# Optimization experiments

Measured on AMD Instinct MI355X. Metric: run time of the kernel, lower is better.

Reference implementation:

```python
import jax, jax.numpy as jnp
import numpy as np

D_MODEL = 1024
N_HEADS = 16
HEAD_DIM = D_MODEL // N_HEADS
B, S = 2, 2048


def setup_inputs() -> dict:
    key = jax.random.key(0)
    ks = jax.random.split(key, 12)
    sd = 1.0 / np.sqrt(D_MODEL)
    inp = {
        "x": jax.random.normal(ks[0], (B, S, D_MODEL), dtype=jnp.float32),
        "rel_bias": jax.random.normal(ks[1], (N_HEADS, S, S), dtype=jnp.float32) * 0.02,
        "attn_mask": jnp.zeros((1, 1, S, S), dtype=jnp.float32),
        # Linear params in torch layout: W [out, in], b [out]
        "Wq": jax.random.normal(ks[2], (D_MODEL, D_MODEL), dtype=jnp.float32) * sd,
        "bq": jnp.zeros((D_MODEL,), dtype=jnp.float32),
        "Wk": jax.random.normal(ks[3], (D_MODEL, D_MODEL), dtype=jnp.float32) * sd,
        "bk": jnp.zeros((D_MODEL,), dtype=jnp.float32),
        "Wv": jax.random.normal(ks[4], (D_MODEL, D_MODEL), dtype=jnp.float32) * sd,
        "bv": jnp.zeros((D_MODEL,), dtype=jnp.float32),
        "Wo": jax.random.normal(ks[5], (D_MODEL, D_MODEL), dtype=jnp.float32) * sd,
        "bo": jnp.zeros((D_MODEL,), dtype=jnp.float32),
    }
    return inp


def _split_heads(t):
    # [B, S, D] -> [B, H, S, Hd]
    b, s, _ = t.shape
    return t.reshape(b, s, N_HEADS, HEAD_DIM).transpose(0, 2, 1, 3)


def reference(x, rel_bias, attn_mask, Wq, bq, Wk, bk, Wv, bv, Wo, bo):
    scale = HEAD_DIM ** (-0.5)
    q = _split_heads(x @ Wq.T + bq)  # [B, H, S, Hd]
    k = _split_heads(x @ Wk.T + bk)
    v = _split_heads(x @ Wv.T + bv)
    scores = jnp.einsum("bhqd,bhkd->bhqk", q, k) * scale
    scores = scores + rel_bias  # [H,S,S] broadcasts over batch
    scores = scores + attn_mask  # [1,1,S,S]
    probs = jax.nn.softmax(scores, axis=-1)
    ctx = jnp.einsum("bhqk,bhkd->bhqd", probs, v)  # [B, H, S, Hd]
    ctx = ctx.transpose(0, 2, 1, 3).reshape(x.shape[0], x.shape[1], D_MODEL)
    return ctx @ Wo.T + bo
```

## Files before the change

### kernel.cpp

```cpp
#include <hip/hip_runtime.h>
#include <hip/hip_bf16.h>
#include <stdint.h>

#define S_LEN 2048
#define DM 1024
#define NH 16
#define HD 64

typedef __bf16 bf16x8 __attribute__((ext_vector_type(8)));
typedef float f32x4 __attribute__((ext_vector_type(4)));
typedef unsigned short u16x4 __attribute__((ext_vector_type(4)));

#if __has_builtin(__builtin_amdgcn_exp2f)
#define EXP2F(x) __builtin_amdgcn_exp2f(x)
#else
#define EXP2F(x) exp2f(x)
#endif

__device__ __forceinline__ unsigned short f2bf(float f){
  union { float f; uint32_t u; } v; v.f = f;
  uint32_t r = v.u + 0x7fffu + ((v.u >> 16) & 1u);
  return (unsigned short)(r >> 16);
}

__device__ __forceinline__ float bf2f(unsigned short u){
  union { uint32_t u; float f; } v; v.u = ((uint32_t)u) << 16;
  return v.f;
}

__device__ __forceinline__ void load_lds16(const void* g, void* l){
  __builtin_amdgcn_global_load_lds((const __attribute__((address_space(1))) void*)g,
                                   (__attribute__((address_space(3))) void*)l, 16, 0, 0);
}

__device__ __forceinline__ f32x4 mfma16(bf16x8 a, bf16x8 b, f32x4 c){
  return __builtin_amdgcn_mfma_f32_16x16x32_bf16(a, b, c, 0, 0, 0);
}

__device__ __forceinline__ bf16x8 lds_swz_read(const unsigned short* base, int row, int cb){
  int addr = (row << 7) + (cb ^ ((row & 7) << 4));
  return *reinterpret_cast<const bf16x8*>(reinterpret_cast<const char*>(base) + addr);
}

__global__ void prep_kernel(const float* __restrict__ x,
                            const float* __restrict__ wq, const float* __restrict__ wk,
                            const float* __restrict__ wv, const float* __restrict__ wo,
                            unsigned short* __restrict__ ws_base){
  long idx = ((long)blockIdx.x * 256 + threadIdx.x) * 4;
  const float* s; unsigned short* d; long off;
  if (idx < (1L << 22)) { s = x; d = ws_base; off = idx; }
  else {
    long r = idx - (1L << 22);
    int wsel = (int)(r >> 20);
    off = r & ((1L << 20) - 1);
    s = wsel == 0 ? wq : wsel == 1 ? wk : wsel == 2 ? wv : wo;
    d = ws_base + (1L << 22) + ((long)wsel << 20);
  }
  float4 f = *reinterpret_cast<const float4*>(s + off);
  u16x4 o;
  o[0] = f2bf(f.x); o[1] = f2bf(f.y); o[2] = f2bf(f.z); o[3] = f2bf(f.w);
  *reinterpret_cast<u16x4*>(d + off) = o;
}

template<int MODE>
__global__ __launch_bounds__(256, 2)
void gemm_bt_kernel(const unsigned short* __restrict__ A,
                    const unsigned short* __restrict__ B0,
                    const unsigned short* __restrict__ B1,
                    const unsigned short* __restrict__ B2,
                    const float* __restrict__ bias0,
                    const float* __restrict__ bias1,
                    const float* __restrict__ bias2,
                    unsigned short* __restrict__ q_out,
                    unsigned short* __restrict__ k_out,
                    unsigned short* __restrict__ vt_out,
                    float* __restrict__ f_out)
{
  __shared__ unsigned short As[128 * 64];
  __shared__ unsigned short Bs[128 * 64];
  const int tid = threadIdx.x;
  const int lane = tid & 63;
  const int w = tid >> 6;
  const int wr = w >> 1, wc = w & 1;
  const int mBase = blockIdx.y * 128;
  int nb = blockIdx.x;
  const unsigned short* Bmat; const float* bias; int mat;
  if constexpr (MODE == 0) {
    mat = nb >> 3;
    nb &= 7;
    Bmat = mat == 0 ? B0 : (mat == 1 ? B1 : B2);
    bias = mat == 0 ? bias0 : (mat == 1 ? bias1 : bias2);
  } else { mat = 0; Bmat = B0; bias = bias0; }
  const int nBase = nb * 128;

  f32x4 acc[4][4] = {};
  const int srow = lane >> 3;
  const int ksrc = ((lane & 7) ^ srow) * 8;
  const unsigned short* ArowBase = A    + (size_t)(mBase + w * 32 + srow) * DM + ksrc;
  const unsigned short* BrowBase = Bmat + (size_t)(nBase + w * 32 + srow) * DM + ksrc;

  for (int kt = 0; kt < 16; ++kt) {
    #pragma unroll
    for (int i = 0; i < 4; ++i) {
      load_lds16(ArowBase + (size_t)(i * 8) * DM + kt * 64, &As[(w * 4 + i) * 512]);
      load_lds16(BrowBase + (size_t)(i * 8) * DM + kt * 64, &Bs[(w * 4 + i) * 512]);
    }
    __syncthreads();
    #pragma unroll
    for (int kk = 0; kk < 2; ++kk) {
      bf16x8 af[4], bfr[4];
      const int cb = kk * 64 + ((lane >> 4) << 4);
      #pragma unroll
      for (int m = 0; m < 4; ++m)
        af[m] = lds_swz_read(As, wr * 64 + m * 16 + (lane & 15), cb);
      #pragma unroll
      for (int n = 0; n < 4; ++n)
        bfr[n] = lds_swz_read(Bs, wc * 64 + n * 16 + (lane & 15), cb);
      #pragma unroll
      for (int m = 0; m < 4; ++m)
        #pragma unroll
        for (int n = 0; n < 4; ++n)
          acc[m][n] = mfma16(af[m], bfr[n], acc[m][n]);
    }
    __syncthreads();
  }

  #pragma unroll
  for (int m = 0; m < 4; ++m) {
    #pragma unroll
    for (int n = 0; n < 4; ++n) {
      const int col = nBase + wc * 64 + n * 16 + (lane & 15);
      const float bv = bias[col];
      const int row0 = mBase + wr * 64 + m * 16 + ((lane >> 4) << 2);
      if constexpr (MODE == 1) {
        #pragma unroll
        for (int j = 0; j < 4; ++j)
          f_out[(size_t)(row0 + j) * DM + col] = acc[m][n][j] + bv;
      } else {
        const int h = col >> 6, d = col & 63;
        if (mat < 2) {
          unsigned short* dst = (mat == 0) ? q_out : k_out;
          #pragma unroll
          for (int j = 0; j < 4; ++j) {
            const int row = row0 + j;
            const int b = row >> 11, s = row & 2047;
            dst[(((size_t)b * NH + h) * S_LEN + s) * HD + d] = f2bf(acc[m][n][j] + bv);
          }
        } else {
          const int b = row0 >> 11, s = row0 & 2047;
          u16x4 pk;
          #pragma unroll
          for (int j = 0; j < 4; ++j) pk[j] = f2bf(acc[m][n][j] + bv);
          *reinterpret_cast<u16x4*>(&vt_out[(((size_t)b * NH + h) * HD + d) * S_LEN + s]) = pk;
        }
      }
    }
  }
}


#define WAITV8 do { asm volatile("s_waitcnt vmcnt(8)" ::: "memory"); } while (0)
#define WAITV2 do { asm volatile("s_waitcnt vmcnt(2)" ::: "memory"); } while (0)
#define WAITV0 do { asm volatile("s_waitcnt vmcnt(0)" ::: "memory"); } while (0)
#define SB0    __builtin_amdgcn_sched_barrier(0)
#define BAR    __builtin_amdgcn_s_barrier()

#define LOAD_RAW(lB) do {                                                              \
    rb0 = *reinterpret_cast<const f32x4*>(bpB + (size_t)(0  + rg) * S_LEN + (lB) + cl4); \
    rb1 = *reinterpret_cast<const f32x4*>(bpB + (size_t)(4  + rg) * S_LEN + (lB) + cl4); \
    rb2 = *reinterpret_cast<const f32x4*>(bpB + (size_t)(8  + rg) * S_LEN + (lB) + cl4); \
    rb3 = *reinterpret_cast<const f32x4*>(bpB + (size_t)(12 + rg) * S_LEN + (lB) + cl4); \
    rm0 = *reinterpret_cast<const f32x4*>(mpB + (size_t)(0  + rg) * S_LEN + (lB) + cl4); \
    rm1 = *reinterpret_cast<const f32x4*>(mpB + (size_t)(4  + rg) * S_LEN + (lB) + cl4); \
    rm2 = *reinterpret_cast<const f32x4*>(mpB + (size_t)(8  + rg) * S_LEN + (lB) + cl4); \
    rm3 = *reinterpret_cast<const f32x4*>(mpB + (size_t)(12 + rg) * S_LEN + (lB) + cl4); \
  } while (0)

#define COMBINE do {                                                                   \
    f32x4 c0_ = (rb0 + rm0) * L2E; f32x4 c1_ = (rb1 + rm1) * L2E;                      \
    f32x4 c2_ = (rb2 + rm2) * L2E; f32x4 c3_ = (rb3 + rm3) * L2E;                      \
    u16x4 p0_, p1_, p2_, p3_;                                                          \
    p0_[0]=f2bf(c0_[0]); p0_[1]=f2bf(c0_[1]); p0_[2]=f2bf(c0_[2]); p0_[3]=f2bf(c0_[3]);\
    p1_[0]=f2bf(c1_[0]); p1_[1]=f2bf(c1_[1]); p1_[2]=f2bf(c1_[2]); p1_[3]=f2bf(c1_[3]);\
    p2_[0]=f2bf(c2_[0]); p2_[1]=f2bf(c2_[1]); p2_[2]=f2bf(c2_[2]); p2_[3]=f2bf(c2_[3]);\
    p3_[0]=f2bf(c3_[0]); p3_[1]=f2bf(c3_[1]); p3_[2]=f2bf(c3_[2]); p3_[3]=f2bf(c3_[3]);\
    char* Pb_ = reinterpret_cast<char*>(Pw_);                                          \
    *reinterpret_cast<u16x4*>(Pb_ + ((0  + rg) << 7) + (cl8 ^ ((0 + rg) << 4))) = p0_; \
    *reinterpret_cast<u16x4*>(Pb_ + ((4  + rg) << 7) + (cl8 ^ ((4 + rg) << 4))) = p1_; \
    *reinterpret_cast<u16x4*>(Pb_ + ((8  + rg) << 7) + (cl8 ^ ((0 + rg) << 4))) = p2_; \
    *reinterpret_cast<u16x4*>(Pb_ + ((12 + rg) << 7) + (cl8 ^ ((4 + rg) << 4))) = p3_; \
    bm0 = *reinterpret_cast<const u16x4*>(Pb_ + (q << 7) + ((0 * 32 + g * 8) ^ qx_));  \
    bm1 = *reinterpret_cast<const u16x4*>(Pb_ + (q << 7) + ((1 * 32 + g * 8) ^ qx_));  \
    bm2 = *reinterpret_cast<const u16x4*>(Pb_ + (q << 7) + ((2 * 32 + g * 8) ^ qx_));  \
    bm3 = *reinterpret_cast<const u16x4*>(Pb_ + (q << 7) + ((3 * 32 + g * 8) ^ qx_));  \
  } while (0)

#define STAGE_K(kvB) \
    load_lds16(Kp + (size_t)((kvB) + w * 8 + srow) * HD + ksrc, &Ks[w * 512])

#define STAGE_V(kvB) \
    load_lds16(Vp + (size_t)(w * 8 + srow) * S_LEN + (kvB) + ksrc, &Vs[w * 512])

#define BIAS_COL(SCN, BMN) do {                                               \
    SCN[0] = SCN[0] * SC + bf2f(BMN[0]);                                      \
    SCN[1] = SCN[1] * SC + bf2f(BMN[1]);                                      \
    SCN[2] = SCN[2] * SC + bf2f(BMN[2]);                                      \
    SCN[3] = SCN[3] * SC + bf2f(BMN[3]);                                      \
    mt_ = fmaxf(mt_, fmaxf(fmaxf(SCN[0], SCN[1]), fmaxf(SCN[2], SCN[3])));    \
  } while (0)

#define EXP_COL(SCN) do {                                                     \
    SCN[0] = EXP2F(SCN[0] - mn_); SCN[1] = EXP2F(SCN[1] - mn_);               \
    SCN[2] = EXP2F(SCN[2] - mn_); SCN[3] = EXP2F(SCN[3] - mn_);               \
  } while (0)

#define PWR_COL(NN, SCN) do {                                                 \
    u16x4 pk_;                                                                \
    pk_[0] = f2bf(SCN[0]); pk_[1] = f2bf(SCN[1]);                             \
    pk_[2] = f2bf(SCN[2]); pk_[3] = f2bf(SCN[3]);                             \
    const int colb_ = ((NN) * 16 + 4 * g) * 2;                                \
    *reinterpret_cast<u16x4*>(                                                \
        reinterpret_cast<char*>(Pw_) + (q << 7) + (colb_ ^ ((q & 7) << 4))) = pk_; \
  } while (0)

#define COMPUTE_TILE do {                                                     \
    f32x4 sc0_, sc1_, sc2_, sc3_;                                             \
    { bf16x8 a_ = lds_swz_read(Ks, 0 * 16 + q, cbq);                          \
      bf16x8 b_ = lds_swz_read(Ks, 0 * 16 + q, 64 + cbq);                     \
      f32x4 z_ = {}; z_ = mfma16(a_, qf0, z_); sc0_ = mfma16(b_, qf1, z_); }  \
    { bf16x8 a_ = lds_swz_read(Ks, 1 * 16 + q, cbq);                          \
      bf16x8 b_ = lds_swz_read(Ks, 1 * 16 + q, 64 + cbq);                     \
      f32x4 z_ = {}; z_ = mfma16(a_, qf0, z_); sc1_ = mfma16(b_, qf1, z_); }  \
    { bf16x8 a_ = lds_swz_read(Ks, 2 * 16 + q, cbq);                          \
      bf16x8 b_ = lds_swz_read(Ks, 2 * 16 + q, 64 + cbq);                     \
      f32x4 z_ = {}; z_ = mfma16(a_, qf0, z_); sc2_ = mfma16(b_, qf1, z_); }  \
    { bf16x8 a_ = lds_swz_read(Ks, 3 * 16 + q, cbq);                          \
      bf16x8 b_ = lds_swz_read(Ks, 3 * 16 + q, 64 + cbq);                     \
      f32x4 z_ = {}; z_ = mfma16(a_, qf0, z_); sc3_ = mfma16(b_, qf1, z_); }  \
    float mt_ = -3.0e38f;                                                     \
    BIAS_COL(sc0_, bm0); BIAS_COL(sc1_, bm1);                                 \
    BIAS_COL(sc2_, bm2); BIAS_COL(sc3_, bm3);                                 \
    mt_ = fmaxf(mt_, __shfl_xor(mt_, 16));                                    \
    mt_ = fmaxf(mt_, __shfl_xor(mt_, 32));                                    \
    const float mn_ = fmaxf(m_run, mt_);                                      \
    const float corr_ = EXP2F(m_run - mn_);                                   \
    m_run = mn_;                                                              \
    EXP_COL(sc0_); EXP_COL(sc1_); EXP_COL(sc2_); EXP_COL(sc3_);               \
    f32x4 ls4_ = sc0_ + sc1_ + sc2_ + sc3_;                                   \
    float ls_ = ls4_[0] + ls4_[1] + ls4_[2] + ls4_[3];                        \
    ls_ += __shfl_xor(ls_, 16);                                               \
    ls_ += __shfl_xor(ls_, 32);                                               \
    l_run = l_run * corr_ + ls_;                                              \
    acc0_ *= corr_; acc1_ *= corr_; acc2_ *= corr_; acc3_ *= corr_;           \
    PWR_COL(0, sc0_); PWR_COL(1, sc1_); PWR_COL(2, sc2_); PWR_COL(3, sc3_);   \
    bf16x8 pf0_ = lds_swz_read(Pw_, q, cbq);                                  \
    bf16x8 pf1_ = lds_swz_read(Pw_, q, 64 + cbq);                             \
    { bf16x8 a_ = lds_swz_read(Vs, 0 * 16 + q, cbq);                          \
      bf16x8 b_ = lds_swz_read(Vs, 0 * 16 + q, 64 + cbq);                     \
      acc0_ = mfma16(a_, pf0_, acc0_); acc0_ = mfma16(b_, pf1_, acc0_); }     \
    { bf16x8 a_ = lds_swz_read(Vs, 1 * 16 + q, cbq);                          \
      bf16x8 b_ = lds_swz_read(Vs, 1 * 16 + q, 64 + cbq);                     \
      acc1_ = mfma16(a_, pf0_, acc1_); acc1_ = mfma16(b_, pf1_, acc1_); }     \
    { bf16x8 a_ = lds_swz_read(Vs, 2 * 16 + q, cbq);                          \
      bf16x8 b_ = lds_swz_read(Vs, 2 * 16 + q, 64 + cbq);                     \
      acc2_ = mfma16(a_, pf0_, acc2_); acc2_ = mfma16(b_, pf1_, acc2_); }     \
    { bf16x8 a_ = lds_swz_read(Vs, 3 * 16 + q, cbq);                          \
      bf16x8 b_ = lds_swz_read(Vs, 3 * 16 + q, 64 + cbq);                     \
      acc3_ = mfma16(a_, pf0_, acc3_); acc3_ = mfma16(b_, pf1_, acc3_); }     \
  } while (0)

__global__ __launch_bounds__(512) __attribute__((amdgpu_waves_per_eu(4, 5)))
void attn_kernel(const unsigned short* __restrict__ Q,
                 const unsigned short* __restrict__ Kmat,
                 const unsigned short* __restrict__ Vt,
                 const float* __restrict__ rel_bias,
                 const float* __restrict__ mask,
                 unsigned short* __restrict__ ctxp0,
                 unsigned short* __restrict__ ctxp1,
                 unsigned short* __restrict__ ctxp2,
                 unsigned short* __restrict__ ctxp3,
                 float* __restrict__ Mbuf,
                 float* __restrict__ Lbuf)
{
  __shared__ unsigned short Ks[64 * 64];
  __shared__ unsigned short Vs[64 * 64];
  __shared__ unsigned short Ps[8][16 * 64];

  const int logical = (blockIdx.x & 7) * 256 + (blockIdx.x >> 3);
  const int s  = logical & 3;
  const int b  = (logical >> 2) & 1;
  const int qt = (logical >> 3) & 15;
  const int h  = logical >> 7;

  const int lane = threadIdx.x & 63, w = threadIdx.x >> 6;
  const int q = lane & 15, g = lane >> 4;
  const int bh = b * NH + h;
  const int qRow = qt * 128 + w * 16;
  const int kv0 = s << 9;
  const unsigned short* Qp = Q + ((size_t)bh * S_LEN + qRow) * HD;
  bf16x8 qf0 = *reinterpret_cast<const bf16x8*>(Qp + (size_t)q * HD + g * 8);
  bf16x8 qf1 = *reinterpret_cast<const bf16x8*>(Qp + (size_t)q * HD + 32 + g * 8);

  const unsigned short* Kp = Kmat + (size_t)bh * S_LEN * HD;
  const unsigned short* Vp = Vt + (size_t)bh * HD * S_LEN;
  const float* bpB = rel_bias + (size_t)h * S_LEN * S_LEN + (size_t)qRow * S_LEN + kv0;
  const float* mpB = mask + (size_t)qRow * S_LEN + kv0;

  float m_run = -3.0e38f, l_run = 0.f;
  f32x4 acc0_ = {}, acc1_ = {}, acc2_ = {}, acc3_ = {};
  f32x4 rb0, rb1, rb2, rb3, rm0, rm1, rm2, rm3;
  u16x4 bm0, bm1, bm2, bm3;

  const float SC  = 0.125f * 1.44269504089f;
  const float L2E = 1.44269504089f;

  const int srow = lane >> 3;
  const int ksrc = ((lane & 7) ^ srow) * 8;
  const int cbq = g << 4;
  const int rg  = lane >> 4;
  const int cl4 = (lane & 15) * 4;
  const int cl8 = (lane & 15) * 8;
  const int qx_ = (q & 7) << 4;
  unsigned short* Pw_ = Ps[w];

  LOAD_RAW(0);
  SB0;

  for (int t = 0; t < 7; ++t) {
    const int kvB = kv0 + t * 64;
    BAR;
    STAGE_K(kvB); STAGE_V(kvB);
    SB0;
    WAITV2; SB0;
    COMBINE;
    LOAD_RAW((t + 1) * 64);
    SB0;
    WAITV8; SB0;
    BAR;
    COMPUTE_TILE;
  }
  {
    const int kvB = kv0 + 7 * 64;
    BAR;
    STAGE_K(kvB); STAGE_V(kvB);
    SB0;
    WAITV2; SB0;
    COMBINE;
    WAITV0; SB0;
    BAR;
    COMPUTE_TILE;
  }

  const float inv = 1.0f / l_run;
  acc0_ *= inv; acc1_ *= inv; acc2_ *= inv; acc3_ *= inv;
  PWR_COL(0, acc0_); PWR_COL(1, acc1_); PWR_COL(2, acc2_); PWR_COL(3, acc3_);
  bf16x8 c0 = lds_swz_read(Pw_, q, g << 4);
  bf16x8 c1 = lds_swz_read(Pw_, q, 64 + (g << 4));
  unsigned short* pbase = (s == 0) ? ctxp0 : (s == 1) ? ctxp1 : (s == 2) ? ctxp2 : ctxp3;
  unsigned short* cp = pbase + ((size_t)(b * S_LEN + qRow + q)) * DM + h * HD;
  *reinterpret_cast<bf16x8*>(cp + 8 * g) = c0;
  *reinterpret_cast<bf16x8*>(cp + 32 + 8 * g) = c1;
  if (g == 0) {
    const int mlIdx = (s << 16) + (bh << 11) + qRow + q;
    Mbuf[mlIdx] = m_run;
    Lbuf[mlIdx] = l_run;
  }
}

__global__ void merge_kernel(const unsigned short* __restrict__ ctxp0,
                             const unsigned short* __restrict__ ctxp1,
                             const unsigned short* __restrict__ ctxp2,
                             const unsigned short* __restrict__ ctxp3,
                             const float* __restrict__ Mbuf,
                             const float* __restrict__ Lbuf,
                             unsigned short* __restrict__ ctx){
  const long e = ((long)blockIdx.x * 256 + threadIdx.x) * 4;
  const int b = (int)(e >> 21);
  const int srow = (int)((e >> 10) & 2047);
  const int d = (int)(e & 1023);
  const int h = d >> 6;
  const int idx = ((b * NH + h) << 11) + srow;
  const float m0 = Mbuf[idx],               m1 = Mbuf[(1 << 16) + idx];
  const float m2 = Mbuf[(2 << 16) + idx],   m3 = Mbuf[(3 << 16) + idx];
  const float l0 = Lbuf[idx],               l1 = Lbuf[(1 << 16) + idx];
  const float l2 = Lbuf[(2 << 16) + idx],   l3 = Lbuf[(3 << 16) + idx];
  const float mm = fmaxf(fmaxf(m0, m1), fmaxf(m2, m3));
  const float w0 = EXP2F(m0 - mm) * l0;
  const float w1 = EXP2F(m1 - mm) * l1;
  const float w2 = EXP2F(m2 - mm) * l2;
  const float w3 = EXP2F(m3 - mm) * l3;
  const float inv = 1.0f / (w0 + w1 + w2 + w3);
  u16x4 c0 = *reinterpret_cast<const u16x4*>(ctxp0 + e);
  u16x4 c1 = *reinterpret_cast<const u16x4*>(ctxp1 + e);
  u16x4 c2 = *reinterpret_cast<const u16x4*>(ctxp2 + e);
  u16x4 c3 = *reinterpret_cast<const u16x4*>(ctxp3 + e);
  u16x4 o;
  #pragma unroll
  for (int j = 0; j < 4; ++j)
    o[j] = f2bf((bf2f(c0[j]) * w0 + bf2f(c1[j]) * w1 +
                 bf2f(c2[j]) * w2 + bf2f(c3[j]) * w3) * inv);
  *reinterpret_cast<u16x4*>(ctx + e) = o;
}

extern "C" void kernel_launch(void* const* d_in, const int* in_sizes, int n_in,
                              void* d_out, int out_size, void* d_ws, size_t ws_size,
                              hipStream_t stream) {
  (void)in_sizes; (void)n_in; (void)out_size; (void)ws_size;
  const float* x  = (const float*)d_in[0];
  const float* rb = (const float*)d_in[1];
  const float* mk = (const float*)d_in[2];
  const float* Wq = (const float*)d_in[3];
  const float* bq = (const float*)d_in[4];
  const float* Wk = (const float*)d_in[5];
  const float* bk = (const float*)d_in[6];
  const float* Wv = (const float*)d_in[7];
  const float* bv = (const float*)d_in[8];
  const float* Wo = (const float*)d_in[9];
  const float* bo = (const float*)d_in[10];
  float* out = (float*)d_out;

  unsigned short* ws  = (unsigned short*)d_ws;
  unsigned short* xb  = ws;
  unsigned short* wqb = ws + (1L << 22);
  unsigned short* wkb = wqb + (1L << 20);
  unsigned short* wvb = wkb + (1L << 20);
  unsigned short* wob = wvb + (1L << 20);
  unsigned short* Qw  = wob + (1L << 20);
  unsigned short* Kw  = Qw + (1L << 22);
  unsigned short* Vtw = Kw + (1L << 22);
  unsigned short* ctx = Vtw + (1L << 22);
  unsigned short* ctxp1 = xb;
  unsigned short* ctxp2 = (unsigned short*)d_out;
  unsigned short* ctxp3 = (unsigned short*)d_out + (1L << 22);
  float* Mb = (float*)wqb;
  float* Lb = (float*)(wqb + (1L << 19));

  prep_kernel<<<8192, 256, 0, stream>>>(x, Wq, Wk, Wv, Wo, ws);
  gemm_bt_kernel<0><<<dim3(24, 32), 256, 0, stream>>>(
      xb, wqb, wkb, wvb, bq, bk, bv, Qw, Kw, Vtw, nullptr);
  attn_kernel<<<2048, 512, 0, stream>>>(Qw, Kw, Vtw, rb, mk, ctx, ctxp1, ctxp2, ctxp3, Mb, Lb);
  merge_kernel<<<4096, 256, 0, stream>>>(ctx, ctxp1, ctxp2, ctxp3, Mb, Lb, ctx);
  gemm_bt_kernel<1><<<dim3(8, 32), 256, 0, stream>>>(
      ctx, wob, nullptr, nullptr, bo, nullptr, nullptr, nullptr, nullptr, nullptr, out);
}
```

Baseline: 199.9 us.

## Double-buffer K/V tiles in LDS to overlap staging with compute

Splits the K and V shared-memory tiles into two buffers and prefetches the next tile's K/V into the alternate buffer while the current tile is computed. The main loop drops from two barriers per iteration to one, and the raw bias/mask loads are issued before the compute step. This is meant to hide global-to-LDS latency behind the MFMA work, at the cost of doubling K/V LDS usage, which may reduce occupancy. The vmcnt wait counts and the ordering of the in-flight LOAD_RAW loads against the LDS-direct loads are delicate.

```diff
diff --git a/kernel.cpp b/kernel.cpp
--- a/kernel.cpp
+++ b/kernel.cpp
@@ -159,7 +159,6 @@
 }
 
 
-#define WAITV8 do { asm volatile("s_waitcnt vmcnt(8)" ::: "memory"); } while (0)
 #define WAITV2 do { asm volatile("s_waitcnt vmcnt(2)" ::: "memory"); } while (0)
 #define WAITV0 do { asm volatile("s_waitcnt vmcnt(0)" ::: "memory"); } while (0)
 #define SB0    __builtin_amdgcn_sched_barrier(0)
@@ -195,11 +194,11 @@
     bm3 = *reinterpret_cast<const u16x4*>(Pb_ + (q << 7) + ((3 * 32 + g * 8) ^ qx_));  \
   } while (0)
 
-#define STAGE_K(kvB) \
-    load_lds16(Kp + (size_t)((kvB) + w * 8 + srow) * HD + ksrc, &Ks[w * 512])
-
-#define STAGE_V(kvB) \
-    load_lds16(Vp + (size_t)(w * 8 + srow) * S_LEN + (kvB) + ksrc, &Vs[w * 512])
+#define STAGE_K(kvB, buf) \
+    load_lds16(Kp + (size_t)((kvB) + w * 8 + srow) * HD + ksrc, &Ks[buf][w * 512])
+
+#define STAGE_V(kvB, buf) \
+    load_lds16(Vp + (size_t)(w * 8 + srow) * S_LEN + (kvB) + ksrc, &Vs[buf][w * 512])
 
 #define BIAS_COL(SCN, BMN) do {                                               \
     SCN[0] = SCN[0] * SC + bf2f(BMN[0]);                                      \
@@ -223,19 +222,21 @@
         reinterpret_cast<char*>(Pw_) + (q << 7) + (colb_ ^ ((q & 7) << 4))) = pk_; \
   } while (0)
 
-#define COMPUTE_TILE do {                                                     \
+#define COMPUTE_TILE(KSB, VSB) do {                                           \
+    const unsigned short* KSB_ = (KSB);                                       \
+    const unsigned short* VSB_ = (VSB);                                       \
     f32x4 sc0_, sc1_, sc2_, sc3_;                                             \
-    { bf16x8 a_ = lds_swz_read(Ks, 0 * 16 + q, cbq);                          \
-      bf16x8 b_ = lds_swz_read(Ks, 0 * 16 + q, 64 + cbq);                     \
+    { bf16x8 a_ = lds_swz_read(KSB_, 0 * 16 + q, cbq);                        \
+      bf16x8 b_ = lds_swz_read(KSB_, 0 * 16 + q, 64 + cbq);                   \
       f32x4 z_ = {}; z_ = mfma16(a_, qf0, z_); sc0_ = mfma16(b_, qf1, z_); }  \
-    { bf16x8 a_ = lds_swz_read(Ks, 1 * 16 + q, cbq);                          \
-      bf16x8 b_ = lds_swz_read(Ks, 1 * 16 + q, 64 + cbq);                     \
+    { bf16x8 a_ = lds_swz_read(KSB_, 1 * 16 + q, cbq);                        \
+      bf16x8 b_ = lds_swz_read(KSB_, 1 * 16 + q, 64 + cbq);                   \
       f32x4 z_ = {}; z_ = mfma16(a_, qf0, z_); sc1_ = mfma16(b_, qf1, z_); }  \
-    { bf16x8 a_ = lds_swz_read(Ks, 2 * 16 + q, cbq);                          \
-      bf16x8 b_ = lds_swz_read(Ks, 2 * 16 + q, 64 + cbq);                     \
+    { bf16x8 a_ = lds_swz_read(KSB_, 2 * 16 + q, cbq);                        \
+      bf16x8 b_ = lds_swz_read(KSB_, 2 * 16 + q, 64 + cbq);                   \
       f32x4 z_ = {}; z_ = mfma16(a_, qf0, z_); sc2_ = mfma16(b_, qf1, z_); }  \
-    { bf16x8 a_ = lds_swz_read(Ks, 3 * 16 + q, cbq);                          \
-      bf16x8 b_ = lds_swz_read(Ks, 3 * 16 + q, 64 + cbq);                     \
+    { bf16x8 a_ = lds_swz_read(KSB_, 3 * 16 + q, cbq);                        \
+      bf16x8 b_ = lds_swz_read(KSB_, 3 * 16 + q, 64 + cbq);                   \
       f32x4 z_ = {}; z_ = mfma16(a_, qf0, z_); sc3_ = mfma16(b_, qf1, z_); }  \
     float mt_ = -3.0e38f;                                                     \
     BIAS_COL(sc0_, bm0); BIAS_COL(sc1_, bm1);                                 \
@@ -255,17 +256,17 @@
     PWR_COL(0, sc0_); PWR_COL(1, sc1_); PWR_COL(2, sc2_); PWR_COL(3, sc3_);   \
     bf16x8 pf0_ = lds_swz_read(Pw_, q, cbq);                                  \
     bf16x8 pf1_ = lds_swz_read(Pw_, q, 64 + cbq);                             \
-    { bf16x8 a_ = lds_swz_read(Vs, 0 * 16 + q, cbq);                          \
-      bf16x8 b_ = lds_swz_read(Vs, 0 * 16 + q, 64 + cbq);                     \
+    { bf16x8 a_ = lds_swz_read(VSB_, 0 * 16 + q, cbq);                        \
+      bf16x8 b_ = lds_swz_read(VSB_, 0 * 16 + q, 64 + cbq);                   \
       acc0_ = mfma16(a_, pf0_, acc0_); acc0_ = mfma16(b_, pf1_, acc0_); }     \
-    { bf16x8 a_ = lds_swz_read(Vs, 1 * 16 + q, cbq);                          \
-      bf16x8 b_ = lds_swz_read(Vs, 1 * 16 + q, 64 + cbq);                     \
+    { bf16x8 a_ = lds_swz_read(VSB_, 1 * 16 + q, cbq);                        \
+      bf16x8 b_ = lds_swz_read(VSB_, 1 * 16 + q, 64 + cbq);                   \
       acc1_ = mfma16(a_, pf0_, acc1_); acc1_ = mfma16(b_, pf1_, acc1_); }     \
-    { bf16x8 a_ = lds_swz_read(Vs, 2 * 16 + q, cbq);                          \
-      bf16x8 b_ = lds_swz_read(Vs, 2 * 16 + q, 64 + cbq);                     \
+    { bf16x8 a_ = lds_swz_read(VSB_, 2 * 16 + q, cbq);                        \
+      bf16x8 b_ = lds_swz_read(VSB_, 2 * 16 + q, 64 + cbq);                   \
       acc2_ = mfma16(a_, pf0_, acc2_); acc2_ = mfma16(b_, pf1_, acc2_); }     \
-    { bf16x8 a_ = lds_swz_read(Vs, 3 * 16 + q, cbq);                          \
-      bf16x8 b_ = lds_swz_read(Vs, 3 * 16 + q, 64 + cbq);                     \
+    { bf16x8 a_ = lds_swz_read(VSB_, 3 * 16 + q, cbq);                        \
+      bf16x8 b_ = lds_swz_read(VSB_, 3 * 16 + q, 64 + cbq);                   \
       acc3_ = mfma16(a_, pf0_, acc3_); acc3_ = mfma16(b_, pf1_, acc3_); }     \
   } while (0)
 
@@ -282,8 +283,8 @@
                  float* __restrict__ Mbuf,
                  float* __restrict__ Lbuf)
 {
-  __shared__ unsigned short Ks[64 * 64];
-  __shared__ unsigned short Vs[64 * 64];
+  __shared__ unsigned short Ks[2][64 * 64];
+  __shared__ unsigned short Vs[2][64 * 64];
   __shared__ unsigned short Ps[8][16 * 64];
 
   const int logical = (blockIdx.x & 7) * 256 + (blockIdx.x >> 3);
@@ -323,32 +324,29 @@
   const int qx_ = (q & 7) << 4;
   unsigned short* Pw_ = Ps[w];
 
+  STAGE_K(kv0, 0); STAGE_V(kv0, 0);
+  SB0;
   LOAD_RAW(0);
   SB0;
-
-  for (int t = 0; t < 7; ++t) {
-    const int kvB = kv0 + t * 64;
-    BAR;
-    STAGE_K(kvB); STAGE_V(kvB);
-    SB0;
-    WAITV2; SB0;
+  WAITV2; SB0;
+  BAR;
+
+  for (int t = 0; t < 8; ++t) {
+    if (t < 7) {
+      const int kvB = kv0 + (t + 1) * 64;
+      STAGE_K(kvB, (t + 1) & 1); STAGE_V(kvB, (t + 1) & 1);
+      SB0;
+      WAITV2; SB0;
+    } else {
+      WAITV0; SB0;
+    }
     COMBINE;
-    LOAD_RAW((t + 1) * 64);
-    SB0;
-    WAITV8; SB0;
-    BAR;
-    COMPUTE_TILE;
-  }
-  {
-    const int kvB = kv0 + 7 * 64;
-    BAR;
-    STAGE_K(kvB); STAGE_V(kvB);
-    SB0;
-    WAITV2; SB0;
-    COMBINE;
-    WAITV0; SB0;
-    BAR;
-    COMPUTE_TILE;
+    if (t < 7) { LOAD_RAW((t + 1) * 64); SB0; }
+    COMPUTE_TILE(Ks[t & 1], Vs[t & 1]);
+    if (t < 7) {
+      WAITV2; SB0;
+      BAR;
+    }
   }
 
   const float inv = 1.0f / l_run;
```

Result: no change. 197.5 us (-1.2%).
